# Optimization experiments

Measured on AMD Instinct MI355X. Metric: run time of the kernel, lower is better.

Reference implementation:

```python
import jax, jax.numpy as jnp
import numpy as np

BUCKETS = 256


def _gru_cell(x, h, W_ih, W_hh, b_ih, b_hh):
    # torch GRUCell math, gate order (r, z, n)
    gi = x @ W_ih.T + b_ih            # [B, 3H]
    gh = h @ W_hh.T + b_hh            # [B, 3H]
    i_r, i_z, i_n = jnp.split(gi, 3, axis=-1)
    h_r, h_z, h_n = jnp.split(gh, 3, axis=-1)
    r = jax.nn.sigmoid(i_r + h_r)
    z = jax.nn.sigmoid(i_z + h_z)
    n = jnp.tanh(i_n + r * h_n)
    return (1.0 - z) * n + z * h


def setup_inputs() -> dict:
    key = jax.random.key(0)
    ks = jax.random.split(key, 10)
    B, T, C, G, H, V = 16, 2000, 128, 512, 512, BUCKETS
    s = 0.1  # keep gates in a sane range
    return {
        "cond": jax.random.normal(ks[0], (B, T, C), jnp.float32),
        "h0": jnp.zeros((B, G), jnp.float32),
        "W_ih": jax.random.normal(ks[1], (3 * G, C), jnp.float32) * s,
        "W_hh": jax.random.normal(ks[2], (3 * G, G), jnp.float32) * s,
        "b_ih": jax.random.normal(ks[3], (3 * G,), jnp.float32) * s,
        "b_hh": jax.random.normal(ks[4], (3 * G,), jnp.float32) * s,
        "W_hid": jax.random.normal(ks[5], (H, G), jnp.float32) * s,
        "b_hid": jax.random.normal(ks[6], (H,), jnp.float32) * s,
        "W_out": jax.random.normal(ks[7], (V, H), jnp.float32) * s,
        "b_out": jax.random.normal(ks[8], (V,), jnp.float32) * s,
        "embedding": jax.random.normal(ks[9], (V, C), jnp.float32) * s,
    }


def reference(cond, h0, W_ih, W_hh, b_ih, b_hh, W_hid, b_hid, W_out, b_out, embedding):
    B, T, C = cond.shape
    keys = jax.random.split(jax.random.key(1), T)
    prev0 = jnp.full((B,), BUCKETS // 2, jnp.int32)  # mid-bucket = mu-law zero

    def step(carry, inp):
        h, prev = carry
        cond_t, k = inp
        x = cond_t + embedding[prev]                  # [B, C]
        h = _gru_cell(x, h, W_ih, W_hh, b_ih, b_hh)   # [B, G]
        hid = jax.nn.relu(h @ W_hid.T + b_hid)        # [B, H]
        logits = hid @ W_out.T + b_out                # [B, V]
        sample = jax.random.categorical(k, logits, axis=-1).astype(jnp.int32)
        return (h, sample), (logits, sample)

    (h_final, _), (logits, samples) = jax.lax.scan(
        step, (h0, prev0), (jnp.swapaxes(cond, 0, 1), keys))
    # logits: [T, B, V] -> [B, T, V]; samples: [T, B] -> [B, T]
    return jnp.swapaxes(logits, 0, 1), jnp.swapaxes(samples, 0, 1), h_final
```

## Files before the change

kernel.cpp:

```cpp
#include <hip/hip_runtime.h>
#include <stdint.h>
#include <math.h>

#define NBLK 128
#define NTHR 256
#define Bn 16
#define Tn 2000
#define Cn 128
#define Gn 512
#define Hn 512
#define Vn 256

#define WS_DBL_BASE 512
#define GRP_STRIDE  6144

#define OUT_SAMP ((size_t)Bn*Tn*Vn)
#define OUT_HF   (OUT_SAMP + (size_t)Bn*Tn)

typedef __attribute__((ext_vector_type(2))) double d2_t;

__device__ __forceinline__ unsigned rotl32(unsigned v, int n) {
  return (v << n) | (v >> (32 - n));
}

__device__ __forceinline__ void threefry2x32(unsigned k0, unsigned k1,
                                             unsigned c0, unsigned c1,
                                             unsigned& o0, unsigned& o1) {
  unsigned ks2 = k0 ^ k1 ^ 0x1BD11BDAu;
  unsigned x0 = c0 + k0;
  unsigned x1 = c1 + k1;
#define TF_R(r) { x0 += x1; x1 = rotl32(x1, r); x1 ^= x0; }
  TF_R(13) TF_R(15) TF_R(26) TF_R(6)
  x0 += k1;  x1 += ks2 + 1u;
  TF_R(17) TF_R(29) TF_R(16) TF_R(24)
  x0 += ks2; x1 += k0 + 2u;
  TF_R(13) TF_R(15) TF_R(26) TF_R(6)
  x0 += k0;  x1 += k1 + 3u;
  TF_R(17) TF_R(29) TF_R(16) TF_R(24)
  x0 += k1;  x1 += ks2 + 4u;
  TF_R(13) TF_R(15) TF_R(26) TF_R(6)
  x0 += ks2; x1 += k0 + 5u;
#undef TF_R
  o0 = x0; o1 = x1;
}

__device__ __forceinline__ double jax_gumbel(unsigned kt0, unsigned kt1,
                                             unsigned f) {
  unsigned r0, r1;
  threefry2x32(kt0, kt1, 0u, f, r0, r1);
  unsigned bits = r0 ^ r1;
  float uf = __uint_as_float((bits >> 9) | 0x3f800000u) - 1.0f;
  if (uf <= 0.f) uf = 1.17549435e-38f;
  return -log(-log((double)uf));
}

__device__ __forceinline__ void stp(double* p, double v, double s) {
  d2_t d; d.x = v; d.y = s;
  asm volatile("global_store_dwordx4 %0, %1, off sc0 sc1"
               :: "v"(p), "v"(d) : "memory");
}
__device__ __forceinline__ void ldp2(const double* p, d2_t& a, d2_t& b) {
  asm volatile("global_load_dwordx4 %0, %2, off sc0 sc1\n\t"
               "global_load_dwordx4 %1, %2, off offset:16 sc0 sc1\n\t"
               "s_waitcnt vmcnt(0)"
               : "=&v"(a), "=&v"(b) : "v"(p) : "memory");
}
__device__ __forceinline__ void ldp8(const double* p0, const double* p1,
                                     const double* p2, const double* p3,
                                     const double* p4, const double* p5,
                                     const double* p6, const double* p7,
                                     d2_t* r) {
  d2_t r0, r1, r2, r3, r4, r5, r6, r7;
  asm volatile(
    "global_load_dwordx4 %[o0], %[a0], off sc0 sc1\n\t"
    "global_load_dwordx4 %[o1], %[a1], off sc0 sc1\n\t"
    "global_load_dwordx4 %[o2], %[a2], off sc0 sc1\n\t"
    "global_load_dwordx4 %[o3], %[a3], off sc0 sc1\n\t"
    "global_load_dwordx4 %[o4], %[a4], off sc0 sc1\n\t"
    "global_load_dwordx4 %[o5], %[a5], off sc0 sc1\n\t"
    "global_load_dwordx4 %[o6], %[a6], off sc0 sc1\n\t"
    "global_load_dwordx4 %[o7], %[a7], off sc0 sc1\n\t"
    "s_waitcnt vmcnt(0)"
    : [o0]"=&v"(r0), [o1]"=&v"(r1), [o2]"=&v"(r2), [o3]"=&v"(r3),
      [o4]"=&v"(r4), [o5]"=&v"(r5), [o6]"=&v"(r6), [o7]"=&v"(r7)
    : [a0]"v"(p0), [a1]"v"(p1), [a2]"v"(p2), [a3]"v"(p3),
      [a4]"v"(p4), [a5]"v"(p5), [a6]"v"(p6), [a7]"v"(p7)
    : "memory");
  r[0]=r0; r[1]=r1; r[2]=r2; r[3]=r3; r[4]=r4; r[5]=r5; r[6]=r6; r[7]=r7;
}

extern "C" __global__ __launch_bounds__(NTHR)
void wavernn_pipe(const float* __restrict__ cond, const float* __restrict__ h0,
                  const float* __restrict__ W_ih, const float* __restrict__ W_hh,
                  const float* __restrict__ b_ih, const float* __restrict__ b_hh,
                  const float* __restrict__ W_hid, const float* __restrict__ b_hid,
                  const float* __restrict__ W_out, const float* __restrict__ b_out,
                  const float* __restrict__ emb,
                  float* __restrict__ out, double* __restrict__ ws) {
  const int tid = threadIdx.x;
  const int blk = blockIdx.x;
  const int g = blk >> 3;
  const int j = blk & 7;
  const int lane = tid & 63, wv = tid >> 6;

  double* G   = ws + WS_DBL_BASE + (size_t)g * GRP_STRIDE;
  double* Hb0 = G;
  double* Hb1 = G + 1024;
  double* PLp = G + 2048;

  __shared__ __attribute__((aligned(32))) double s_x[Cn];
  __shared__ __attribute__((aligned(32))) double s_h[Gn];
  __shared__ __attribute__((aligned(32))) double s_hid[64];
  __shared__ double s_hn[64], s_in[64], s_z[64];
  __shared__ double s_part[4][64];
  __shared__ double s_gum[256];
  __shared__ float  s_cond[Cn];
  __shared__ double s_pv[4];
  __shared__ int    s_pi[4];

  const double bout_reg = (double)b_out[tid];

  const double* plA0 = PLp + 2 * tid;
  const double* plA1 = plA0 + 512;
  const double* plA2 = plA0 + 1024;
  const double* plA3 = plA0 + 1536;
  const double* plA4 = plA0 + 2048;
  const double* plA5 = plA0 + 2560;
  const double* plA6 = plA0 + 3072;
  const double* plA7 = plA0 + 3584;

  if (tid < 64) stp(&Hb0[2 * (j * 64 + tid)],
                    (double)h0[(size_t)g * Gn + j * 64 + tid], 1.0);
  if (tid < Cn) s_x[tid] = (double)cond[(size_t)g * Tn * Cn + tid]
                         + (double)emb[128 * Cn + tid];
  {
    d2_t a, b; int guard = 0;
    do { ldp2(Hb0 + 4 * tid, a, b); }
    while ((a.y != 1.0 || b.y != 1.0) && ++guard < 2000000);
    s_h[2 * tid] = a.x; s_h[2 * tid + 1] = b.x;
  }
  __syncthreads();

  for (int t = 0; t < Tn; ++t) {
    double* hnxt = (t & 1) ? Hb0 : Hb1;

    double ha0 = 0., ha1 = 0., ha2 = 0., ha3 = 0.;
    if (wv <= 2) {
      const int row = wv * 512 + j * 64 + lane;
      const float4* wh = (const float4*)(W_hh + (size_t)row * Gn);
      const double4* h4 = (const double4*)s_h;
#pragma unroll 8
      for (int k = 0; k < Gn / 4; ++k) {
        float4 w = wh[k]; double4 hv = h4[k];
        ha0 = fma((double)w.x, hv.x, ha0); ha1 = fma((double)w.y, hv.y, ha1);
        ha2 = fma((double)w.z, hv.z, ha2); ha3 = fma((double)w.w, hv.w, ha3);
      }
      if (wv == 2)
        s_hn[lane] = ((ha0 + ha1) + (ha2 + ha3)) + (double)b_hh[row];
    } else {
      const int c0 = 2 * lane;
      s_cond[c0]     = cond[((size_t)g * Tn + t) * Cn + c0];
      s_cond[c0 + 1] = cond[((size_t)g * Tn + t) * Cn + c0 + 1];
      if (t > 0) {
        unsigned kt0, kt1;
        threefry2x32(0u, 1u, 0u, (unsigned)(t - 1), kt0, kt1);
#pragma unroll
        for (int i = 0; i < 4; ++i) {
          int v = 4 * lane + i;
          s_gum[v] = jax_gumbel(kt0, kt1, (unsigned)(g * Vn + v));
        }
      }
    }

    if (t > 0) {
      const double exP = (double)t;
      double l[8];
      {
        d2_t r[8]; int guard = 0;
        for (;;) {
          ldp8(plA0, plA1, plA2, plA3, plA4, plA5, plA6, plA7, r);
          bool ok = (r[0].y == exP) & (r[1].y == exP) & (r[2].y == exP)
                  & (r[3].y == exP) & (r[4].y == exP) & (r[5].y == exP)
                  & (r[6].y == exP) & (r[7].y == exP);
          if (ok || ++guard > 2000000) {
            l[0]=r[0].x; l[1]=r[1].x; l[2]=r[2].x; l[3]=r[3].x;
            l[4]=r[4].x; l[5]=r[5].x; l[6]=r[6].x; l[7]=r[7].x;
            break;
          }
        }
      }
      const int v = tid;
      double logit = ((((((((l[0] + l[1]) + l[2]) + l[3]) + l[4]) + l[5])
                       + l[6]) + l[7])) + bout_reg;
      if (j == 0)
        out[(size_t)g * Tn * Vn + (size_t)(t - 1) * Vn + v] = (float)logit;
      double bv = logit + s_gum[v];
      int bi = v;
#pragma unroll
      for (int off = 1; off < 64; off <<= 1) {
        double ov = __shfl_xor(bv, off, 64);
        int oi = __shfl_xor(bi, off, 64);
        if (ov > bv || (ov == bv && oi < bi)) { bv = ov; bi = oi; }
      }
      if (lane == 0) { s_pv[wv] = bv; s_pi[wv] = bi; }
      __syncthreads();
      double fv = s_pv[0]; int fi = s_pi[0];
#pragma unroll
      for (int w = 1; w < 4; ++w) {
        double ov = s_pv[w]; int oi = s_pi[w];
        if (ov > fv || (ov == fv && oi < fi)) { fv = ov; fi = oi; }
      }
      const int samp = fi;
      if (tid == 0 && j == 0)
        out[OUT_SAMP + (size_t)g * Tn + (t - 1)] = (float)samp;
      if (tid < Cn)
        s_x[tid] = (double)s_cond[tid] + (double)emb[(size_t)samp * Cn + tid];
      __syncthreads();
    } else {
      __syncthreads();
    }

    double r_reg = 0.;
    if (wv <= 1) {
      const int row = wv * 512 + j * 64 + lane;
      const float4* wi = (const float4*)(W_ih + (size_t)row * Cn);
      const double4* x4 = (const double4*)s_x;
      double xa0 = 0., xa1 = 0., xa2 = 0., xa3 = 0.;
#pragma unroll 8
      for (int k = 0; k < Cn / 4; ++k) {
        float4 w = wi[k]; double4 xv = x4[k];
        xa0 = fma((double)w.x, xv.x, xa0); xa1 = fma((double)w.y, xv.y, xa1);
        xa2 = fma((double)w.z, xv.z, xa2); xa3 = fma((double)w.w, xv.w, xa3);
      }
      double gi = ((xa0 + xa1) + (xa2 + xa3)) + (double)b_ih[row];
      double gh = ((ha0 + ha1) + (ha2 + ha3)) + (double)b_hh[row];
      double pre = gi + gh;
      double sig = 1.0 / (1.0 + exp(-pre));
      if (wv == 0) r_reg = sig; else s_z[lane] = sig;
    } else if (wv == 3) {
      const int row = 1024 + j * 64 + lane;
      const float4* wi = (const float4*)(W_ih + (size_t)row * Cn);
      const double4* x4 = (const double4*)s_x;
      double a0 = 0., a1 = 0., a2 = 0., a3 = 0.;
#pragma unroll 8
      for (int k = 0; k < Cn / 4; ++k) {
        float4 w = wi[k]; double4 xv = x4[k];
        a0 = fma((double)w.x, xv.x, a0); a1 = fma((double)w.y, xv.y, a1);
        a2 = fma((double)w.z, xv.z, a2); a3 = fma((double)w.w, xv.w, a3);
      }
      s_in[lane] = ((a0 + a1) + (a2 + a3)) + (double)b_ih[row];
    }
    __syncthreads();

    if (wv == 0) {
      double z = s_z[lane];
      double n = tanh(s_in[lane] + r_reg * s_hn[lane]);
      double hv = (1.0 - z) * n + z * s_h[j * 64 + lane];
      stp(&hnxt[2 * (j * 64 + lane)], hv, (double)(t + 2));
    }
    __syncthreads();
    {
      const double exH = (double)(t + 2);
      d2_t a, b; int guard = 0;
      do { ldp2(hnxt + 4 * tid, a, b); }
      while ((a.y != exH || b.y != exH) && ++guard < 2000000);
      s_h[2 * tid] = a.x; s_h[2 * tid + 1] = b.x;
    }
    __syncthreads();
    if (t == Tn - 1 && j == 0) {
      out[OUT_HF + (size_t)g * Gn + tid] = (float)s_h[tid];
      out[OUT_HF + (size_t)g * Gn + tid + 256] = (float)s_h[tid + 256];
    }

    {
      const int row = j * 64 + lane;
      const float4* wr = (const float4*)(W_hid + (size_t)row * Gn + wv * 128);
      const double4* hh = (const double4*)(s_h + wv * 128);
      double a0 = 0., a1 = 0., a2 = 0., a3 = 0.;
#pragma unroll 8
      for (int k = 0; k < 32; ++k) {
        float4 w = wr[k]; double4 hv = hh[k];
        a0 = fma((double)w.x, hv.x, a0); a1 = fma((double)w.y, hv.y, a1);
        a2 = fma((double)w.z, hv.z, a2); a3 = fma((double)w.w, hv.w, a3);
      }
      s_part[wv][lane] = (a0 + a1) + (a2 + a3);
    }
    __syncthreads();
    if (tid < 64) {
      double acc = (s_part[0][tid] + s_part[1][tid])
                 + (s_part[2][tid] + s_part[3][tid])
                 + (double)b_hid[j * 64 + tid];
      s_hid[tid] = acc > 0.0 ? acc : 0.0;
    }
    __syncthreads();
    {
      const int v = tid;
      const float4* wr = (const float4*)(W_out + (size_t)v * Hn + j * 64);
      const double4* hh = (const double4*)s_hid;
      double a0 = 0., a1 = 0., a2 = 0., a3 = 0.;
#pragma unroll 8
      for (int k = 0; k < 16; ++k) {
        float4 w = wr[k]; double4 hv = hh[k];
        a0 = fma((double)w.x, hv.x, a0); a1 = fma((double)w.y, hv.y, a1);
        a2 = fma((double)w.z, hv.z, a2); a3 = fma((double)w.w, hv.w, a3);
      }
      stp(&PLp[2 * (j * 256 + v)], (a0 + a1) + (a2 + a3), (double)(t + 1));
    }
  }

  {
    const double exP = (double)Tn;
    double l[8];
    {
      d2_t r[8]; int guard = 0;
      for (;;) {
        ldp8(plA0, plA1, plA2, plA3, plA4, plA5, plA6, plA7, r);
        bool ok = (r[0].y == exP) & (r[1].y == exP) & (r[2].y == exP)
                & (r[3].y == exP) & (r[4].y == exP) & (r[5].y == exP)
                & (r[6].y == exP) & (r[7].y == exP);
        if (ok || ++guard > 2000000) {
          l[0]=r[0].x; l[1]=r[1].x; l[2]=r[2].x; l[3]=r[3].x;
          l[4]=r[4].x; l[5]=r[5].x; l[6]=r[6].x; l[7]=r[7].x;
          break;
        }
      }
    }
    const int v = tid;
    double logit = ((((((((l[0] + l[1]) + l[2]) + l[3]) + l[4]) + l[5])
                     + l[6]) + l[7])) + bout_reg;
    if (j == 0)
      out[(size_t)g * Tn * Vn + (size_t)(Tn - 1) * Vn + v] = (float)logit;
    unsigned kt0, kt1;
    threefry2x32(0u, 1u, 0u, (unsigned)(Tn - 1), kt0, kt1);
    double gum = jax_gumbel(kt0, kt1, (unsigned)(g * Vn + v));
    double bv = logit + gum;
    int bi = v;
#pragma unroll
    for (int off = 1; off < 64; off <<= 1) {
      double ov = __shfl_xor(bv, off, 64);
      int oi = __shfl_xor(bi, off, 64);
      if (ov > bv || (ov == bv && oi < bi)) { bv = ov; bi = oi; }
    }
    if (lane == 0) { s_pv[wv] = bv; s_pi[wv] = bi; }
    __syncthreads();
    double fv = s_pv[0]; int fi = s_pi[0];
#pragma unroll
    for (int w = 1; w < 4; ++w) {
      double ov = s_pv[w]; int oi = s_pi[w];
      if (ov > fv || (ov == fv && oi < fi)) { fv = ov; fi = oi; }
    }
    if (tid == 0 && j == 0)
      out[OUT_SAMP + (size_t)g * Tn + (Tn - 1)] = (float)fi;
  }
}

extern "C" void kernel_launch(void* const* d_in, const int* in_sizes, int n_in,
                              void* d_out, int out_size, void* d_ws, size_t ws_size,
                              hipStream_t stream) {
  const float* cond  = (const float*)d_in[0];
  const float* h0    = (const float*)d_in[1];
  const float* W_ih  = (const float*)d_in[2];
  const float* W_hh  = (const float*)d_in[3];
  const float* b_ih  = (const float*)d_in[4];
  const float* b_hh  = (const float*)d_in[5];
  const float* W_hid = (const float*)d_in[6];
  const float* b_hid = (const float*)d_in[7];
  const float* W_out = (const float*)d_in[8];
  const float* b_out = (const float*)d_in[9];
  const float* emb   = (const float*)d_in[10];

  hipMemsetAsync(d_ws, 0, 4096, stream);
  hipLaunchKernelGGL(wavernn_pipe, dim3(NBLK), dim3(NTHR), 0, stream,
                     cond, h0, W_ih, W_hh, b_ih, b_hh, W_hid, b_hid,
                     W_out, b_out, emb, (float*)d_out, (double*)d_ws);
}
```

Measured before the change: 45.17 ms.

## Merge pairs of slice blocks into 512-thread blocks, halving inter-block sync

Each block of 512 threads now handles two 64-row slices of the GRU and output projection, so each batch row uses 4 blocks instead of 8 and the grid drops to 64 blocks. This cuts the number of blocks exchanging hidden state and partial logits through global-memory flag polling per step. Only the first 256 threads poll and reduce the logits, and an extra block barrier is added before that reduction. The cost is more work per block, with each block now streaming weight rows for two slices.

```diff
diff --git a/kernel.cpp b/kernel.cpp
--- a/kernel.cpp
+++ b/kernel.cpp
@@ -2,8 +2,8 @@
 #include <stdint.h>
 #include <math.h>
 
-#define NBLK 128
-#define NTHR 256
+#define NBLK 64
+#define NTHR 512
 #define Bn 16
 #define Tn 2000
 #define Cn 128
@@ -89,7 +89,7 @@
   r[0]=r0; r[1]=r1; r[2]=r2; r[3]=r3; r[4]=r4; r[5]=r5; r[6]=r6; r[7]=r7;
 }
 
-extern "C" __global__ __launch_bounds__(NTHR)
+extern "C" __global__ __launch_bounds__(NTHR, 1)
 void wavernn_pipe(const float* __restrict__ cond, const float* __restrict__ h0,
                   const float* __restrict__ W_ih, const float* __restrict__ W_hh,
                   const float* __restrict__ b_ih, const float* __restrict__ b_hh,
@@ -99,9 +99,12 @@
                   float* __restrict__ out, double* __restrict__ ws) {
   const int tid = threadIdx.x;
   const int blk = blockIdx.x;
-  const int g = blk >> 3;
-  const int j = blk & 7;
+  const int g = blk >> 2;
+  const int b = blk & 3;
   const int lane = tid & 63, wv = tid >> 6;
+  const int half = wv >> 2;
+  const int wl = wv & 3;
+  const int j = 2 * b + half;
 
   double* G   = ws + WS_DBL_BASE + (size_t)g * GRP_STRIDE;
   double* Hb0 = G;
@@ -110,17 +113,17 @@
 
   __shared__ __attribute__((aligned(32))) double s_x[Cn];
   __shared__ __attribute__((aligned(32))) double s_h[Gn];
-  __shared__ __attribute__((aligned(32))) double s_hid[64];
-  __shared__ double s_hn[64], s_in[64], s_z[64];
-  __shared__ double s_part[4][64];
+  __shared__ __attribute__((aligned(32))) double s_hid[128];
+  __shared__ double s_hn[2][64], s_in[2][64], s_z[2][64];
+  __shared__ double s_part[2][4][64];
   __shared__ double s_gum[256];
   __shared__ float  s_cond[Cn];
   __shared__ double s_pv[4];
   __shared__ int    s_pi[4];
 
-  const double bout_reg = (double)b_out[tid];
-
-  const double* plA0 = PLp + 2 * tid;
+  const double bout_reg = (double)b_out[tid & 255];
+
+  const double* plA0 = PLp + 2 * (tid & 255);
   const double* plA1 = plA0 + 512;
   const double* plA2 = plA0 + 1024;
   const double* plA3 = plA0 + 1536;
@@ -129,15 +132,15 @@
   const double* plA6 = plA0 + 3072;
   const double* plA7 = plA0 + 3584;
 
-  if (tid < 64) stp(&Hb0[2 * (j * 64 + tid)],
-                    (double)h0[(size_t)g * Gn + j * 64 + tid], 1.0);
+  if (tid < 128) stp(&Hb0[2 * (b * 128 + tid)],
+                     (double)h0[(size_t)g * Gn + b * 128 + tid], 1.0);
   if (tid < Cn) s_x[tid] = (double)cond[(size_t)g * Tn * Cn + tid]
                          + (double)emb[128 * Cn + tid];
-  {
-    d2_t a, b; int guard = 0;
-    do { ldp2(Hb0 + 4 * tid, a, b); }
-    while ((a.y != 1.0 || b.y != 1.0) && ++guard < 2000000);
-    s_h[2 * tid] = a.x; s_h[2 * tid + 1] = b.x;
+  if (tid < 256) {
+    d2_t a, c; int guard = 0;
+    do { ldp2(Hb0 + 4 * tid, a, c); }
+    while ((a.y != 1.0 || c.y != 1.0) && ++guard < 2000000);
+    s_h[2 * tid] = a.x; s_h[2 * tid + 1] = c.x;
   }
   __syncthreads();
 
@@ -145,8 +148,8 @@
     double* hnxt = (t & 1) ? Hb0 : Hb1;
 
     double ha0 = 0., ha1 = 0., ha2 = 0., ha3 = 0.;
-    if (wv <= 2) {
-      const int row = wv * 512 + j * 64 + lane;
+    if (wl <= 2) {
+      const int row = wl * 512 + j * 64 + lane;
       const float4* wh = (const float4*)(W_hh + (size_t)row * Gn);
       const double4* h4 = (const double4*)s_h;
 #pragma unroll 8
@@ -155,25 +158,168 @@
         ha0 = fma((double)w.x, hv.x, ha0); ha1 = fma((double)w.y, hv.y, ha1);
         ha2 = fma((double)w.z, hv.z, ha2); ha3 = fma((double)w.w, hv.w, ha3);
       }
-      if (wv == 2)
-        s_hn[lane] = ((ha0 + ha1) + (ha2 + ha3)) + (double)b_hh[row];
+      if (wl == 2)
+        s_hn[half][lane] = ((ha0 + ha1) + (ha2 + ha3)) + (double)b_hh[row];
     } else {
-      const int c0 = 2 * lane;
-      s_cond[c0]     = cond[((size_t)g * Tn + t) * Cn + c0];
-      s_cond[c0 + 1] = cond[((size_t)g * Tn + t) * Cn + c0 + 1];
+      if (half == 0) {
+        const int c0 = 2 * lane;
+        s_cond[c0]     = cond[((size_t)g * Tn + t) * Cn + c0];
+        s_cond[c0 + 1] = cond[((size_t)g * Tn + t) * Cn + c0 + 1];
+      }
       if (t > 0) {
         unsigned kt0, kt1;
         threefry2x32(0u, 1u, 0u, (unsigned)(t - 1), kt0, kt1);
 #pragma unroll
-        for (int i = 0; i < 4; ++i) {
-          int v = 4 * lane + i;
+        for (int i = 0; i < 2; ++i) {
+          int v = half * 128 + 2 * lane + i;
           s_gum[v] = jax_gumbel(kt0, kt1, (unsigned)(g * Vn + v));
         }
       }
     }
 
     if (t > 0) {
-      const double exP = (double)t;
+      __syncthreads();
+      if (tid < 256) {
+        const double exP = (double)t;
+        double l[8];
+        {
+          d2_t r[8]; int guard = 0;
+          for (;;) {
+            ldp8(plA0, plA1, plA2, plA3, plA4, plA5, plA6, plA7, r);
+            bool ok = (r[0].y == exP) & (r[1].y == exP) & (r[2].y == exP)
+                    & (r[3].y == exP) & (r[4].y == exP) & (r[5].y == exP)
+                    & (r[6].y == exP) & (r[7].y == exP);
+            if (ok || ++guard > 2000000) {
+              l[0]=r[0].x; l[1]=r[1].x; l[2]=r[2].x; l[3]=r[3].x;
+              l[4]=r[4].x; l[5]=r[5].x; l[6]=r[6].x; l[7]=r[7].x;
+              break;
+            }
+          }
+        }
+        const int v = tid;
+        double logit = ((((((((l[0] + l[1]) + l[2]) + l[3]) + l[4]) + l[5])
+                         + l[6]) + l[7])) + bout_reg;
+        if (b == 0)
+          out[(size_t)g * Tn * Vn + (size_t)(t - 1) * Vn + v] = (float)logit;
+        double bv = logit + s_gum[v];
+        int bi = v;
+#pragma unroll
+        for (int off = 1; off < 64; off <<= 1) {
+          double ov = __shfl_xor(bv, off, 64);
+          int oi = __shfl_xor(bi, off, 64);
+          if (ov > bv || (ov == bv && oi < bi)) { bv = ov; bi = oi; }
+        }
+        if (lane == 0) { s_pv[wv] = bv; s_pi[wv] = bi; }
+      }
+      __syncthreads();
+      double fv = s_pv[0]; int fi = s_pi[0];
+#pragma unroll
+      for (int w = 1; w < 4; ++w) {
+        double ov = s_pv[w]; int oi = s_pi[w];
+        if (ov > fv || (ov == fv && oi < fi)) { fv = ov; fi = oi; }
+      }
+      const int samp = fi;
+      if (tid == 0 && b == 0)
+        out[OUT_SAMP + (size_t)g * Tn + (t - 1)] = (float)samp;
+      if (tid < Cn)
+        s_x[tid] = (double)s_cond[tid] + (double)emb[(size_t)samp * Cn + tid];
+      __syncthreads();
+    } else {
+      __syncthreads();
+    }
+
+    double r_reg = 0.;
+    if (wl <= 1) {
+      const int row = wl * 512 + j * 64 + lane;
+      const float4* wi = (const float4*)(W_ih + (size_t)row * Cn);
+      const double4* x4 = (const double4*)s_x;
+      double xa0 = 0., xa1 = 0., xa2 = 0., xa3 = 0.;
+#pragma unroll 8
+      for (int k = 0; k < Cn / 4; ++k) {
+        float4 w = wi[k]; double4 xv = x4[k];
+        xa0 = fma((double)w.x, xv.x, xa0); xa1 = fma((double)w.y, xv.y, xa1);
+        xa2 = fma((double)w.z, xv.z, xa2); xa3 = fma((double)w.w, xv.w, xa3);
+      }
+      double gi = ((xa0 + xa1) + (xa2 + xa3)) + (double)b_ih[row];
+      double gh = ((ha0 + ha1) + (ha2 + ha3)) + (double)b_hh[row];
+      double pre = gi + gh;
+      double sig = 1.0 / (1.0 + exp(-pre));
+      if (wl == 0) r_reg = sig; else s_z[half][lane] = sig;
+    } else if (wl == 3) {
+      const int row = 1024 + j * 64 + lane;
+      const float4* wi = (const float4*)(W_ih + (size_t)row * Cn);
+      const double4* x4 = (const double4*)s_x;
+      double a0 = 0., a1 = 0., a2 = 0., a3 = 0.;
+#pragma unroll 8
+      for (int k = 0; k < Cn / 4; ++k) {
+        float4 w = wi[k]; double4 xv = x4[k];
+        a0 = fma((double)w.x, xv.x, a0); a1 = fma((double)w.y, xv.y, a1);
+        a2 = fma((double)w.z, xv.z, a2); a3 = fma((double)w.w, xv.w, a3);
+      }
+      s_in[half][lane] = ((a0 + a1) + (a2 + a3)) + (double)b_ih[row];
+    }
+    __syncthreads();
+
+    if (wl == 0) {
+      double z = s_z[half][lane];
+      double n = tanh(s_in[half][lane] + r_reg * s_hn[half][lane]);
+      double hv = (1.0 - z) * n + z * s_h[j * 64 + lane];
+      stp(&hnxt[2 * (j * 64 + lane)], hv, (double)(t + 2));
+    }
+    __syncthreads();
+    if (tid < 256) {
+      const double exH = (double)(t + 2);
+      d2_t a, c; int guard = 0;
+      do { ldp2(hnxt + 4 * tid, a, c); }
+      while ((a.y != exH || c.y != exH) && ++guard < 2000000);
+      s_h[2 * tid] = a.x; s_h[2 * tid + 1] = c.x;
+    }
+    __syncthreads();
+    if (t == Tn - 1 && b == 0)
+      out[OUT_HF + (size_t)g * Gn + tid] = (float)s_h[tid];
+
+    {
+      const int row = j * 64 + lane;
+      const float4* wr = (const float4*)(W_hid + (size_t)row * Gn + wl * 128);
+      const double4* hh = (const double4*)(s_h + wl * 128);
+      double a0 = 0., a1 = 0., a2 = 0., a3 = 0.;
+#pragma unroll 8
+      for (int k = 0; k < 32; ++k) {
+        float4 w = wr[k]; double4 hv = hh[k];
+        a0 = fma((double)w.x, hv.x, a0); a1 = fma((double)w.y, hv.y, a1);
+        a2 = fma((double)w.z, hv.z, a2); a3 = fma((double)w.w, hv.w, a3);
+      }
+      s_part[half][wl][lane] = (a0 + a1) + (a2 + a3);
+    }
+    __syncthreads();
+    if (tid < 128) {
+      const int hf = tid >> 6, l = tid & 63;
+      double acc = (s_part[hf][0][l] + s_part[hf][1][l])
+                 + (s_part[hf][2][l] + s_part[hf][3][l])
+                 + (double)b_hid[(2 * b + hf) * 64 + l];
+      s_hid[tid] = acc > 0.0 ? acc : 0.0;
+    }
+    __syncthreads();
+    {
+      const int vv = tid & 255;
+      const int hf = tid >> 8;
+      const int jj = 2 * b + hf;
+      const float4* wr = (const float4*)(W_out + (size_t)vv * Hn + jj * 64);
+      const double4* hh = (const double4*)(s_hid + hf * 64);
+      double a0 = 0., a1 = 0., a2 = 0., a3 = 0.;
+#pragma unroll 8
+      for (int k = 0; k < 16; ++k) {
+        float4 w = wr[k]; double4 hv = hh[k];
+        a0 = fma((double)w.x, hv.x, a0); a1 = fma((double)w.y, hv.y, a1);
+        a2 = fma((double)w.z, hv.z, a2); a3 = fma((double)w.w, hv.w, a3);
+      }
+      stp(&PLp[2 * (jj * 256 + vv)], (a0 + a1) + (a2 + a3), (double)(t + 1));
+    }
+  }
+
+  {
+    if (tid < 256) {
+      const double exP = (double)Tn;
       double l[8];
       {
         d2_t r[8]; int guard = 0;
@@ -192,9 +338,12 @@
       const int v = tid;
       double logit = ((((((((l[0] + l[1]) + l[2]) + l[3]) + l[4]) + l[5])
                        + l[6]) + l[7])) + bout_reg;
-      if (j == 0)
-        out[(size_t)g * Tn * Vn + (size_t)(t - 1) * Vn + v] = (float)logit;
-      double bv = logit + s_gum[v];
+      if (b == 0)
+        out[(size_t)g * Tn * Vn + (size_t)(Tn - 1) * Vn + v] = (float)logit;
+      unsigned kt0, kt1;
+      threefry2x32(0u, 1u, 0u, (unsigned)(Tn - 1), kt0, kt1);
+      double gum = jax_gumbel(kt0, kt1, (unsigned)(g * Vn + v));
+      double bv = logit + gum;
       int bi = v;
 #pragma unroll
       for (int off = 1; off < 64; off <<= 1) {
@@ -203,145 +352,7 @@
         if (ov > bv || (ov == bv && oi < bi)) { bv = ov; bi = oi; }
       }
       if (lane == 0) { s_pv[wv] = bv; s_pi[wv] = bi; }
-      __syncthreads();
-      double fv = s_pv[0]; int fi = s_pi[0];
-#pragma unroll
-      for (int w = 1; w < 4; ++w) {
-        double ov = s_pv[w]; int oi = s_pi[w];
-        if (ov > fv || (ov == fv && oi < fi)) { fv = ov; fi = oi; }
-      }
-      const int samp = fi;
-      if (tid == 0 && j == 0)
-        out[OUT_SAMP + (size_t)g * Tn + (t - 1)] = (float)samp;
-      if (tid < Cn)
-        s_x[tid] = (double)s_cond[tid] + (double)emb[(size_t)samp * Cn + tid];
-      __syncthreads();
-    } else {
-      __syncthreads();
-    }
-
-    double r_reg = 0.;
-    if (wv <= 1) {
-      const int row = wv * 512 + j * 64 + lane;
-      const float4* wi = (const float4*)(W_ih + (size_t)row * Cn);
-      const double4* x4 = (const double4*)s_x;
-      double xa0 = 0., xa1 = 0., xa2 = 0., xa3 = 0.;
-#pragma unroll 8
-      for (int k = 0; k < Cn / 4; ++k) {
-        float4 w = wi[k]; double4 xv = x4[k];
-        xa0 = fma((double)w.x, xv.x, xa0); xa1 = fma((double)w.y, xv.y, xa1);
-        xa2 = fma((double)w.z, xv.z, xa2); xa3 = fma((double)w.w, xv.w, xa3);
-      }
-      double gi = ((xa0 + xa1) + (xa2 + xa3)) + (double)b_ih[row];
-      double gh = ((ha0 + ha1) + (ha2 + ha3)) + (double)b_hh[row];
-      double pre = gi + gh;
-      double sig = 1.0 / (1.0 + exp(-pre));
-      if (wv == 0) r_reg = sig; else s_z[lane] = sig;
-    } else if (wv == 3) {
-      const int row = 1024 + j * 64 + lane;
-      const float4* wi = (const float4*)(W_ih + (size_t)row * Cn);
-      const double4* x4 = (const double4*)s_x;
-      double a0 = 0., a1 = 0., a2 = 0., a3 = 0.;
-#pragma unroll 8
-      for (int k = 0; k < Cn / 4; ++k) {
-        float4 w = wi[k]; double4 xv = x4[k];
-        a0 = fma((double)w.x, xv.x, a0); a1 = fma((double)w.y, xv.y, a1);
-        a2 = fma((double)w.z, xv.z, a2); a3 = fma((double)w.w, xv.w, a3);
-      }
-      s_in[lane] = ((a0 + a1) + (a2 + a3)) + (double)b_ih[row];
-    }
-    __syncthreads();
-
-    if (wv == 0) {
-      double z = s_z[lane];
-      double n = tanh(s_in[lane] + r_reg * s_hn[lane]);
-      double hv = (1.0 - z) * n + z * s_h[j * 64 + lane];
-      stp(&hnxt[2 * (j * 64 + lane)], hv, (double)(t + 2));
-    }
-    __syncthreads();
-    {
-      const double exH = (double)(t + 2);
-      d2_t a, b; int guard = 0;
-      do { ldp2(hnxt + 4 * tid, a, b); }
-      while ((a.y != exH || b.y != exH) && ++guard < 2000000);
-      s_h[2 * tid] = a.x; s_h[2 * tid + 1] = b.x;
-    }
-    __syncthreads();
-    if (t == Tn - 1 && j == 0) {
-      out[OUT_HF + (size_t)g * Gn + tid] = (float)s_h[tid];
-      out[OUT_HF + (size_t)g * Gn + tid + 256] = (float)s_h[tid + 256];
-    }
-
-    {
-      const int row = j * 64 + lane;
-      const float4* wr = (const float4*)(W_hid + (size_t)row * Gn + wv * 128);
-      const double4* hh = (const double4*)(s_h + wv * 128);
-      double a0 = 0., a1 = 0., a2 = 0., a3 = 0.;
-#pragma unroll 8
-      for (int k = 0; k < 32; ++k) {
-        float4 w = wr[k]; double4 hv = hh[k];
-        a0 = fma((double)w.x, hv.x, a0); a1 = fma((double)w.y, hv.y, a1);
-        a2 = fma((double)w.z, hv.z, a2); a3 = fma((double)w.w, hv.w, a3);
-      }
-      s_part[wv][lane] = (a0 + a1) + (a2 + a3);
-    }
-    __syncthreads();
-    if (tid < 64) {
-      double acc = (s_part[0][tid] + s_part[1][tid])
-                 + (s_part[2][tid] + s_part[3][tid])
-                 + (double)b_hid[j * 64 + tid];
-      s_hid[tid] = acc > 0.0 ? acc : 0.0;
-    }
-    __syncthreads();
-    {
-      const int v = tid;
-      const float4* wr = (const float4*)(W_out + (size_t)v * Hn + j * 64);
-      const double4* hh = (const double4*)s_hid;
-      double a0 = 0., a1 = 0., a2 = 0., a3 = 0.;
-#pragma unroll 8
-      for (int k = 0; k < 16; ++k) {
-        float4 w = wr[k]; double4 hv = hh[k];
-        a0 = fma((double)w.x, hv.x, a0); a1 = fma((double)w.y, hv.y, a1);
-        a2 = fma((double)w.z, hv.z, a2); a3 = fma((double)w.w, hv.w, a3);
-      }
-      stp(&PLp[2 * (j * 256 + v)], (a0 + a1) + (a2 + a3), (double)(t + 1));
-    }
-  }
-
-  {
-    const double exP = (double)Tn;
-    double l[8];
-    {
-      d2_t r[8]; int guard = 0;
-      for (;;) {
-        ldp8(plA0, plA1, plA2, plA3, plA4, plA5, plA6, plA7, r);
-        bool ok = (r[0].y == exP) & (r[1].y == exP) & (r[2].y == exP)
-                & (r[3].y == exP) & (r[4].y == exP) & (r[5].y == exP)
-                & (r[6].y == exP) & (r[7].y == exP);
-        if (ok || ++guard > 2000000) {
-          l[0]=r[0].x; l[1]=r[1].x; l[2]=r[2].x; l[3]=r[3].x;
-          l[4]=r[4].x; l[5]=r[5].x; l[6]=r[6].x; l[7]=r[7].x;
-          break;
-        }
-      }
-    }
-    const int v = tid;
-    double logit = ((((((((l[0] + l[1]) + l[2]) + l[3]) + l[4]) + l[5])
-                     + l[6]) + l[7])) + bout_reg;
-    if (j == 0)
-      out[(size_t)g * Tn * Vn + (size_t)(Tn - 1) * Vn + v] = (float)logit;
-    unsigned kt0, kt1;
-    threefry2x32(0u, 1u, 0u, (unsigned)(Tn - 1), kt0, kt1);
-    double gum = jax_gumbel(kt0, kt1, (unsigned)(g * Vn + v));
-    double bv = logit + gum;
-    int bi = v;
-#pragma unroll
-    for (int off = 1; off < 64; off <<= 1) {
-      double ov = __shfl_xor(bv, off, 64);
-      int oi = __shfl_xor(bi, off, 64);
-      if (ov > bv || (ov == bv && oi < bi)) { bv = ov; bi = oi; }
-    }
-    if (lane == 0) { s_pv[wv] = bv; s_pi[wv] = bi; }
+    }
     __syncthreads();
     double fv = s_pv[0]; int fi = s_pi[0];
 #pragma unroll
@@ -349,7 +360,7 @@
       double ov = s_pv[w]; int oi = s_pi[w];
       if (ov > fv || (ov == fv && oi < fi)) { fv = ov; fi = oi; }
     }
-    if (tid == 0 && j == 0)
+    if (tid == 0 && b == 0)
       out[OUT_SAMP + (size_t)g * Tn + (Tn - 1)] = (float)fi;
   }
 }
```

Measured after the change: 83.65 ms. 1.85x slower.
